# Performance work log

Measured on AMD Instinct MI355X. Metric: run time of the kernel, lower is better.

## Reference

```python
import jax, jax.numpy as jnp
import numpy as np

N_NODES = 100000
N_EDGES = 3200000
IN_DIM = 20
HIDDEN = 4096
OUT_DIM = 2
BN_EPS = 1e-5


def setup_inputs() -> dict:
    key = jax.random.key(0)
    ks = jax.random.split(key, 6)
    node_feature = jax.random.normal(ks[0], (N_NODES, IN_DIM), dtype=jnp.float32)
    edge_index = jax.random.randint(ks[1], (2, N_EDGES), 0, N_NODES, dtype=jnp.int64)
    gcn_w = jax.random.normal(ks[2], (IN_DIM, HIDDEN), dtype=jnp.float32) * (1.0 / np.sqrt(IN_DIM))
    gcn_b = jax.random.normal(ks[3], (HIDDEN,), dtype=jnp.float32) * 0.01
    bn_gamma = jnp.ones((HIDDEN,), dtype=jnp.float32)
    bn_beta = jnp.zeros((HIDDEN,), dtype=jnp.float32)
    lin_w = jax.random.normal(ks[4], (HIDDEN, OUT_DIM), dtype=jnp.float32) * (1.0 / np.sqrt(HIDDEN))
    lin_b = jnp.zeros((OUT_DIM,), dtype=jnp.float32)
    return {"node_feature": node_feature, "edge_index": edge_index,
            "gcn_w": gcn_w, "gcn_b": gcn_b, "bn_gamma": bn_gamma,
            "bn_beta": bn_beta, "lin_w": lin_w, "lin_b": lin_b}


def reference(node_feature, edge_index, gcn_w, gcn_b, bn_gamma, bn_beta, lin_w, lin_b):
    n = node_feature.shape[0]
    # --- GCNConv: add self loops, symmetric degree normalization ---
    loop = jnp.arange(n, dtype=edge_index.dtype)
    row = jnp.concatenate([edge_index[0], loop])  # source nodes
    col = jnp.concatenate([edge_index[1], loop])  # destination nodes
    deg = jax.ops.segment_sum(jnp.ones(col.shape[0], dtype=node_feature.dtype), col, num_segments=n)
    dinv = jnp.where(deg > 0, jax.lax.rsqrt(deg), 0.0)
    norm = dinv[row] * dinv[col]  # [E+N]
    # Aggregate in the small input dim (20), then transform: scatter(norm*x)W == scatter(norm*xW)
    msgs = node_feature[row] * norm[:, None]              # [E+N, in]
    agg = jax.ops.segment_sum(msgs, col, num_segments=n)  # [N, in]
    h = agg @ gcn_w + gcn_b                                # [N, hidden]
    # --- BatchNorm1d (training-mode batch stats, biased variance) ---
    mean = jnp.mean(h, axis=0)
    var = jnp.mean(jnp.square(h - mean), axis=0)
    h = (h - mean) * jax.lax.rsqrt(var + BN_EPS) * bn_gamma + bn_beta
    rsu_embedding = h[0:1]  # [1, hidden]
    # --- Linear -> ReLU -> Softmax(dim=1) ---
    logits = jax.nn.relu(h @ lin_w + lin_b)  # [N, out]
    action_prob = jax.nn.softmax(logits, axis=1)
    return action_prob, rsu_embedding
```

## Files before the change

kernel.cpp:

```cpp
#include <hip/hip_runtime.h>

#define N_NODES 100000
#define N_EDGES 3200000
#define IN_DIM 20
#define HIDDEN 4096
#define OUT_DIM 2
#define BN_EPS 1e-5f

#define NB 1000
#define NPB 100
#define BIN_CHUNK 8192
#define BIN_NWG ((N_EDGES + BIN_CHUNK - 1) / BIN_CHUNK)

#define WS_NEED 34415616ull

__global__ void k_deg(const int* __restrict__ ei, int* __restrict__ deg) {
    int e = blockIdx.x * blockDim.x + threadIdx.x;
    if (e < N_EDGES) atomicAdd(&deg[ei[N_EDGES + e]], 1);
}

__global__ void k_dinv(const int* __restrict__ deg, float* __restrict__ dinv) {
    int i = blockIdx.x * blockDim.x + threadIdx.x;
    if (i < N_NODES) dinv[i] = rsqrtf((float)(deg[i] + 1));
}

__global__ void k_bh(const int* __restrict__ deg, int* __restrict__ bh) {
    __shared__ int lds[128];
    int b = blockIdx.x, t = threadIdx.x;
    int v = (t < NPB) ? deg[b * NPB + t] : 0;
    lds[t] = v;
    __syncthreads();
    for (int off = 64; off > 0; off >>= 1) {
        if (t < off) lds[t] += lds[t + off];
        __syncthreads();
    }
    if (t == 0) bh[b] = lds[0];
}

__global__ void k_scan_bo(const int* __restrict__ bh, int* __restrict__ bo,
                          int* __restrict__ gcur) {
    __shared__ int lds[256];
    int t = threadIdx.x;
    int base = t * 4;
    int v0 = (base + 0 < NB) ? bh[base + 0] : 0;
    int v1 = (base + 1 < NB) ? bh[base + 1] : 0;
    int v2 = (base + 2 < NB) ? bh[base + 2] : 0;
    int v3 = (base + 3 < NB) ? bh[base + 3] : 0;
    int tsum = v0 + v1 + v2 + v3;
    int x = tsum;
    lds[t] = x;
    __syncthreads();
    for (int off = 1; off < 256; off <<= 1) {
        int y = (t >= off) ? lds[t - off] : 0;
        __syncthreads();
        x += y;
        lds[t] = x;
        __syncthreads();
    }
    int ex = x - tsum;
    if (base + 0 < NB) { bo[base + 0] = ex;                 gcur[base + 0] = ex; }
    if (base + 1 < NB) { bo[base + 1] = ex + v0;            gcur[base + 1] = ex + v0; }
    if (base + 2 < NB) { bo[base + 2] = ex + v0 + v1;       gcur[base + 2] = ex + v0 + v1; }
    if (base + 3 < NB) { bo[base + 3] = ex + v0 + v1 + v2;  gcur[base + 3] = ex + v0 + v1 + v2; }
    if (t == 255) bo[NB] = x;
}

__global__ void k_bin(const int* __restrict__ ei, int* __restrict__ gcur,
                      int2* __restrict__ rec) {
    __shared__ int lh[NB];
    __shared__ int loff[NB];
    int t = threadIdx.x;
    int ebase = blockIdx.x * BIN_CHUNK;
    int eend = min(ebase + BIN_CHUNK, N_EDGES);
    for (int b = t; b < NB; b += 256) lh[b] = 0;
    __syncthreads();
    for (int e = ebase + t; e < eend; e += 256) {
        int c = ei[N_EDGES + e];
        atomicAdd(&lh[c / NPB], 1);
    }
    __syncthreads();
    for (int b = t; b < NB; b += 256) {
        int cnt = lh[b];
        loff[b] = cnt ? atomicAdd(&gcur[b], cnt) : 0;
        lh[b] = 0;
    }
    __syncthreads();
    for (int e = ebase + t; e < eend; e += 256) {
        int r = ei[e];
        int c = ei[N_EDGES + e];
        int b = c / NPB;
        int p = loff[b] + atomicAdd(&lh[b], 1);
        rec[p] = make_int2(r, c);
    }
}

__global__ void k_agg(const int2* __restrict__ rec, const int* __restrict__ bo,
                      const float* __restrict__ nf, const float* __restrict__ dinv,
                      float* __restrict__ agg) {
    __shared__ float tile[NPB * IN_DIM];
    __shared__ float sdinv[NPB];
    int b = blockIdx.x;
    int t = threadIdx.x;
    int base = b * NPB;
    if (t < NPB) sdinv[t] = dinv[base + t];
    __syncthreads();
    const float4* nf4 = (const float4*)nf;
    float4* tile4 = (float4*)tile;
    for (int idx = t; idx < NPB * IN_DIM / 4; idx += 256) {
        int j = idx / 5;
        float d = sdinv[j];
        float s = d * d;
        float4 v = nf4[base * 5 + idx];
        v.x *= s; v.y *= s; v.z *= s; v.w *= s;
        tile4[idx] = v;
    }
    __syncthreads();
    int rend = bo[b + 1];
    for (int i = bo[b] + t; i < rend; i += 256) {
        int2 rc = rec[i];
        int r = rc.x;
        int cl = rc.y - base;
        float w = dinv[r] * sdinv[cl];
        const float4* nfr = nf4 + r * 5;
        float* dst = tile + cl * IN_DIM;
#pragma unroll
        for (int g = 0; g < 5; g++) {
            float4 v = nfr[g];
            atomicAdd(&dst[g * 4 + 0], v.x * w);
            atomicAdd(&dst[g * 4 + 1], v.y * w);
            atomicAdd(&dst[g * 4 + 2], v.z * w);
            atomicAdd(&dst[g * 4 + 3], v.w * w);
        }
    }
    __syncthreads();
    float4* agg4 = (float4*)agg;
    for (int idx = t; idx < NPB * IN_DIM / 4; idx += 256)
        agg4[base * 5 + idx] = tile4[idx];
}

__global__ void k_moments3(const float* __restrict__ agg, float* __restrict__ S1,
                           float* __restrict__ S2) {
    int y = blockIdx.y;
    int a0 = 3 * y, a1 = 3 * y + 1, a2 = 3 * y + 2;
    float acc0[IN_DIM], acc1[IN_DIM], acc2[IN_DIM];
#pragma unroll
    for (int b = 0; b < IN_DIM; b++) { acc0[b] = 0.f; acc1[b] = 0.f; acc2[b] = 0.f; }
    int stride = gridDim.x * blockDim.x;
    for (int i = blockIdx.x * blockDim.x + threadIdx.x; i < N_NODES; i += stride) {
        const float* row = agg + i * IN_DIM;
        float v[IN_DIM];
#pragma unroll
        for (int b = 0; b < IN_DIM; b++) v[b] = row[b];
        float va0 = row[a0];
        float va1 = row[a1];
        float va2 = (a2 < IN_DIM) ? row[a2] : 1.0f;
#pragma unroll
        for (int b = 0; b < IN_DIM; b++) {
            acc0[b] += va0 * v[b];
            acc1[b] += va1 * v[b];
            acc2[b] += va2 * v[b];
        }
    }
#pragma unroll
    for (int b = 0; b < IN_DIM; b++) {
        float r0 = acc0[b], r1 = acc1[b], r2 = acc2[b];
#pragma unroll
        for (int s = 32; s > 0; s >>= 1) {
            r0 += __shfl_down(r0, s);
            r1 += __shfl_down(r1, s);
            r2 += __shfl_down(r2, s);
        }
        acc0[b] = r0; acc1[b] = r1; acc2[b] = r2;
    }
    if ((threadIdx.x & 63) == 0) {
        float* d0 = S2 + a0 * IN_DIM;
        float* d1 = S2 + a1 * IN_DIM;
        float* d2 = (a2 < IN_DIM) ? (S2 + a2 * IN_DIM) : S1;
#pragma unroll
        for (int b = 0; b < IN_DIM; b++) {
            atomicAdd(&d0[b], acc0[b]);
            atomicAdd(&d1[b], acc1[b]);
            atomicAdd(&d2[b], acc2[b]);
        }
    }
}

__global__ void k_stats(const float* __restrict__ S1, const float* __restrict__ S2,
                        const float* __restrict__ agg, float* __restrict__ mean,
                        float* __restrict__ cov, float* __restrict__ agg0c) {
    int t = threadIdx.x;
    const float invn = 1.0f / (float)N_NODES;
    if (t < IN_DIM) {
        float m = S1[t] * invn;
        mean[t] = m;
        agg0c[t] = agg[t] - m;
    }
    __syncthreads();
    for (int idx = t; idx < IN_DIM * IN_DIM; idx += 64) {
        int a = idx / IN_DIM, b = idx - a * IN_DIM;
        cov[idx] = S2[idx] * invn - mean[a] * mean[b];
    }
}

__global__ void k_prep(const float* __restrict__ gcn_w, const float* __restrict__ gamma,
                       const float* __restrict__ beta, const float* __restrict__ lin_w,
                       const float* __restrict__ cov, const float* __restrict__ agg0c,
                       float* __restrict__ W2, float* __restrict__ dvec,
                       float* __restrict__ out_rsu) {
    __shared__ float scov[IN_DIM * IN_DIM];
    __shared__ float sa0[IN_DIM];
    int tid = threadIdx.x;
    for (int idx = tid; idx < IN_DIM * IN_DIM; idx += blockDim.x) scov[idx] = cov[idx];
    if (tid < IN_DIM) sa0[tid] = agg0c[tid];
    __syncthreads();
    int j = blockIdx.x * blockDim.x + tid;

    float wcol[IN_DIM];
#pragma unroll
    for (int t = 0; t < IN_DIM; t++) wcol[t] = gcn_w[t * HIDDEN + j];

    float var = 0.f;
#pragma unroll
    for (int t = 0; t < IN_DIM; t++) {
        float s = 0.f;
#pragma unroll
        for (int u = 0; u < IN_DIM; u++) s += scov[t * IN_DIM + u] * wcol[u];
        var += wcol[t] * s;
    }
    float aj = gamma[j] * rsqrtf(var + BN_EPS);

    float e0 = 0.f;
#pragma unroll
    for (int t = 0; t < IN_DIM; t++) e0 += sa0[t] * wcol[t];
    out_rsu[j] = e0 * aj + beta[j];

    float lw0 = lin_w[2 * j], lw1 = lin_w[2 * j + 1];
    float bj = beta[j];
    float vals[42];
#pragma unroll
    for (int t = 0; t < IN_DIM; t++) {
        vals[2 * t]     = wcol[t] * aj * lw0;
        vals[2 * t + 1] = wcol[t] * aj * lw1;
    }
    vals[40] = bj * lw0;
    vals[41] = bj * lw1;
#pragma unroll
    for (int q = 0; q < 42; q++) {
        float v = vals[q];
#pragma unroll
        for (int s = 32; s > 0; s >>= 1) v += __shfl_down(v, s);
        if ((tid & 63) == 0) {
            if (q < 40) atomicAdd(&W2[q], v);
            else        atomicAdd(&dvec[q - 40], v);
        }
    }
}

__global__ void k_final(const float* __restrict__ agg, const float* __restrict__ mean,
                        const float* __restrict__ W2, const float* __restrict__ dvec,
                        const float* __restrict__ lin_b, float* __restrict__ out) {
    int i = blockIdx.x * blockDim.x + threadIdx.x;
    if (i >= N_NODES) return;
    float d0 = dvec[0] + lin_b[0];
    float d1 = dvec[1] + lin_b[1];
#pragma unroll
    for (int t = 0; t < IN_DIM; t++) {
        float v = agg[i * IN_DIM + t] - mean[t];
        d0 += v * W2[2 * t];
        d1 += v * W2[2 * t + 1];
    }
    float l0 = fmaxf(d0, 0.f), l1 = fmaxf(d1, 0.f);
    float m = fmaxf(l0, l1);
    float e0 = expf(l0 - m), e1 = expf(l1 - m);
    float inv = 1.f / (e0 + e1);
    out[2 * i]     = e0 * inv;
    out[2 * i + 1] = e1 * inv;
}

__global__ void k_agginit(const float* __restrict__ nf, const float* __restrict__ dinv,
                          float* __restrict__ agg) {
    int t = blockIdx.x * blockDim.x + threadIdx.x;
    if (t < N_NODES * IN_DIM) {
        int i = t / IN_DIM;
        float d = dinv[i];
        agg[t] = nf[t] * d * d;
    }
}

__global__ void k_scatter(const int* __restrict__ ei, const float* __restrict__ nf,
                          const float* __restrict__ dinv, float* __restrict__ agg) {
    int t = blockIdx.x * blockDim.x + threadIdx.x;
    if (t >= N_EDGES * IN_DIM) return;
    int e = t / IN_DIM;
    int f = t - e * IN_DIM;
    int r = ei[e];
    int c = ei[N_EDGES + e];
    float w = dinv[r] * dinv[c];
    atomicAdd(&agg[c * IN_DIM + f], nf[r * IN_DIM + f] * w);
}

extern "C" void kernel_launch(void* const* d_in, const int* in_sizes, int n_in,
                              void* d_out, int out_size, void* d_ws, size_t ws_size,
                              hipStream_t stream) {
    const float* nf    = (const float*)d_in[0];
    const int*   ei    = (const int*)d_in[1];
    const float* gcn_w = (const float*)d_in[2];
    const float* gamma = (const float*)d_in[4];
    const float* beta  = (const float*)d_in[5];
    const float* lin_w = (const float*)d_in[6];
    const float* lin_b = (const float*)d_in[7];
    float* out = (float*)d_out;

    char* ws = (char*)d_ws;
    int*   deg  = (int*)(ws + 0);
    float* dinv = (float*)(ws + 400000);
    float* agg  = (float*)(ws + 800000);
    int*   bh   = (int*)(ws + 8800000);
    int*   bo   = (int*)(ws + 8804000);
    int*   gcur = (int*)(ws + 8808004);
    float* S1   = (float*)(ws + 8812004);
    float* S2   = (float*)(ws + 8812084);
    float* mean = (float*)(ws + 8813684);
    float* cov  = (float*)(ws + 8813764);
    float* a0c  = (float*)(ws + 8815364);
    float* W2   = (float*)(ws + 8815444);
    float* dvec = (float*)(ws + 8815604);
    int2*  rec  = (int2*)(ws + 8815616);

    hipMemsetAsync(deg, 0, 400000, stream);
    hipMemsetAsync(S1, 0, 3608, stream);

    k_deg<<<(N_EDGES + 255) / 256, 256, 0, stream>>>(ei, deg);
    k_dinv<<<(N_NODES + 255) / 256, 256, 0, stream>>>(deg, dinv);

    if (ws_size >= WS_NEED) {
        k_bh<<<NB, 128, 0, stream>>>(deg, bh);
        k_scan_bo<<<1, 256, 0, stream>>>(bh, bo, gcur);
        k_bin<<<BIN_NWG, 256, 0, stream>>>(ei, gcur, rec);
        k_agg<<<NB, 256, 0, stream>>>(rec, bo, nf, dinv, agg);
    } else {
        k_agginit<<<(N_NODES * IN_DIM + 255) / 256, 256, 0, stream>>>(nf, dinv, agg);
        k_scatter<<<(N_EDGES * IN_DIM + 255) / 256, 256, 0, stream>>>(ei, nf, dinv, agg);
    }

    dim3 gm(32, 7);
    k_moments3<<<gm, 256, 0, stream>>>(agg, S1, S2);
    k_stats<<<1, 64, 0, stream>>>(S1, S2, agg, mean, cov, a0c);
    k_prep<<<HIDDEN / 256, 256, 0, stream>>>(gcn_w, gamma, beta, lin_w, cov, a0c, W2,
                                             dvec, out + 2 * N_NODES);
    k_final<<<(N_NODES + 255) / 256, 256, 0, stream>>>(agg, mean, W2, dvec, lin_b, out);
}
```

Baseline: 704.9 us.

## Prescale node features by dinv, pack edge records, enlarge agg/bin blocks

Adds a kernel that writes node features pre-multiplied by their source dinv, so the aggregation no longer gathers dinv[r] per edge. The post-sum multiply by the destination dinv moves to the write-out. Edge records shrink from int2 to a packed 32-bit value (source<<7 | local column), which halves record traffic in binning and aggregation. Block sizes for bin and agg grow, and the moments grid is widened. The cost is an extra pass over the features and extra workspace.

```diff
diff --git a/kernel.cpp b/kernel.cpp
--- a/kernel.cpp
+++ b/kernel.cpp
@@ -10,9 +10,11 @@
 #define NB 1000
 #define NPB 100
 #define BIN_CHUNK 8192
+#define BIN_THREADS 512
 #define BIN_NWG ((N_EDGES + BIN_CHUNK - 1) / BIN_CHUNK)
-
-#define WS_NEED 34415616ull
+#define AGG_THREADS 1024
+
+#define WS_NEED 29615616ull
 
 __global__ void k_deg(const int* __restrict__ ei, int* __restrict__ deg) {
     int e = blockIdx.x * blockDim.x + threadIdx.x;
@@ -22,6 +24,21 @@
 __global__ void k_dinv(const int* __restrict__ deg, float* __restrict__ dinv) {
     int i = blockIdx.x * blockDim.x + threadIdx.x;
     if (i < N_NODES) dinv[i] = rsqrtf((float)(deg[i] + 1));
+}
+
+__global__ void k_nfs(const float* __restrict__ nf, const float* __restrict__ dinv,
+                      float* __restrict__ nfs) {
+    int i = blockIdx.x * blockDim.x + threadIdx.x;
+    if (i >= N_NODES) return;
+    float d = dinv[i];
+    const float4* s = (const float4*)nf + i * 5;
+    float4* o = (float4*)nfs + i * 5;
+#pragma unroll
+    for (int g = 0; g < 5; g++) {
+        float4 v = s[g];
+        v.x *= d; v.y *= d; v.z *= d; v.w *= d;
+        o[g] = v;
+    }
 }
 
 __global__ void k_bh(const int* __restrict__ deg, int* __restrict__ bh) {
@@ -66,36 +83,34 @@
 }
 
 __global__ void k_bin(const int* __restrict__ ei, int* __restrict__ gcur,
-                      int2* __restrict__ rec) {
+                      unsigned int* __restrict__ rec) {
     __shared__ int lh[NB];
     __shared__ int loff[NB];
     int t = threadIdx.x;
     int ebase = blockIdx.x * BIN_CHUNK;
     int eend = min(ebase + BIN_CHUNK, N_EDGES);
-    for (int b = t; b < NB; b += 256) lh[b] = 0;
-    __syncthreads();
-    for (int e = ebase + t; e < eend; e += 256) {
-        int c = ei[N_EDGES + e];
-        atomicAdd(&lh[c / NPB], 1);
-    }
-    __syncthreads();
-    for (int b = t; b < NB; b += 256) {
+    for (int b = t; b < NB; b += BIN_THREADS) lh[b] = 0;
+    __syncthreads();
+    for (int e = ebase + t; e < eend; e += BIN_THREADS)
+        atomicAdd(&lh[ei[N_EDGES + e] / NPB], 1);
+    __syncthreads();
+    for (int b = t; b < NB; b += BIN_THREADS) {
         int cnt = lh[b];
         loff[b] = cnt ? atomicAdd(&gcur[b], cnt) : 0;
         lh[b] = 0;
     }
     __syncthreads();
-    for (int e = ebase + t; e < eend; e += 256) {
+    for (int e = ebase + t; e < eend; e += BIN_THREADS) {
         int r = ei[e];
         int c = ei[N_EDGES + e];
         int b = c / NPB;
         int p = loff[b] + atomicAdd(&lh[b], 1);
-        rec[p] = make_int2(r, c);
-    }
-}
-
-__global__ void k_agg(const int2* __restrict__ rec, const int* __restrict__ bo,
-                      const float* __restrict__ nf, const float* __restrict__ dinv,
+        rec[p] = ((unsigned int)r << 7) | (unsigned int)(c - b * NPB);
+    }
+}
+
+__global__ void k_agg(const unsigned int* __restrict__ rec, const int* __restrict__ bo,
+                      const float* __restrict__ nfs, const float* __restrict__ dinv,
                       float* __restrict__ agg) {
     __shared__ float tile[NPB * IN_DIM];
     __shared__ float sdinv[NPB];
@@ -103,39 +118,36 @@
     int t = threadIdx.x;
     int base = b * NPB;
     if (t < NPB) sdinv[t] = dinv[base + t];
-    __syncthreads();
-    const float4* nf4 = (const float4*)nf;
+    const float4* nfs4 = (const float4*)nfs;
     float4* tile4 = (float4*)tile;
-    for (int idx = t; idx < NPB * IN_DIM / 4; idx += 256) {
+    for (int idx = t; idx < NPB * IN_DIM / 4; idx += AGG_THREADS)
+        tile4[idx] = nfs4[base * 5 + idx];
+    __syncthreads();
+    int rend = bo[b + 1];
+    for (int i = bo[b] + t; i < rend; i += AGG_THREADS) {
+        unsigned int v = rec[i];
+        int r = (int)(v >> 7);
+        int cl = (int)(v & 127u);
+        const float4* nfr = nfs4 + r * 5;
+        float* dst = tile + cl * IN_DIM;
+#pragma unroll
+        for (int g = 0; g < 5; g++) {
+            float4 x = nfr[g];
+            atomicAdd(&dst[g * 4 + 0], x.x);
+            atomicAdd(&dst[g * 4 + 1], x.y);
+            atomicAdd(&dst[g * 4 + 2], x.z);
+            atomicAdd(&dst[g * 4 + 3], x.w);
+        }
+    }
+    __syncthreads();
+    float4* agg4 = (float4*)agg;
+    for (int idx = t; idx < NPB * IN_DIM / 4; idx += AGG_THREADS) {
         int j = idx / 5;
-        float d = sdinv[j];
-        float s = d * d;
-        float4 v = nf4[base * 5 + idx];
-        v.x *= s; v.y *= s; v.z *= s; v.w *= s;
-        tile4[idx] = v;
-    }
-    __syncthreads();
-    int rend = bo[b + 1];
-    for (int i = bo[b] + t; i < rend; i += 256) {
-        int2 rc = rec[i];
-        int r = rc.x;
-        int cl = rc.y - base;
-        float w = dinv[r] * sdinv[cl];
-        const float4* nfr = nf4 + r * 5;
-        float* dst = tile + cl * IN_DIM;
-#pragma unroll
-        for (int g = 0; g < 5; g++) {
-            float4 v = nfr[g];
-            atomicAdd(&dst[g * 4 + 0], v.x * w);
-            atomicAdd(&dst[g * 4 + 1], v.y * w);
-            atomicAdd(&dst[g * 4 + 2], v.z * w);
-            atomicAdd(&dst[g * 4 + 3], v.w * w);
-        }
-    }
-    __syncthreads();
-    float4* agg4 = (float4*)agg;
-    for (int idx = t; idx < NPB * IN_DIM / 4; idx += 256)
-        agg4[base * 5 + idx] = tile4[idx];
+        float s = sdinv[j];
+        float4 x = tile4[idx];
+        x.x *= s; x.y *= s; x.z *= s; x.w *= s;
+        agg4[base * 5 + idx] = x;
+    }
 }
 
 __global__ void k_moments3(const float* __restrict__ agg, float* __restrict__ S1,
@@ -325,7 +337,8 @@
     float* a0c  = (float*)(ws + 8815364);
     float* W2   = (float*)(ws + 8815444);
     float* dvec = (float*)(ws + 8815604);
-    int2*  rec  = (int2*)(ws + 8815616);
+    unsigned int* rec = (unsigned int*)(ws + 8815616);
+    float* nfs  = (float*)(ws + 21615616);
 
     hipMemsetAsync(deg, 0, 400000, stream);
     hipMemsetAsync(S1, 0, 3608, stream);
@@ -334,16 +347,17 @@
     k_dinv<<<(N_NODES + 255) / 256, 256, 0, stream>>>(deg, dinv);
 
     if (ws_size >= WS_NEED) {
+        k_nfs<<<(N_NODES + 255) / 256, 256, 0, stream>>>(nf, dinv, nfs);
         k_bh<<<NB, 128, 0, stream>>>(deg, bh);
         k_scan_bo<<<1, 256, 0, stream>>>(bh, bo, gcur);
-        k_bin<<<BIN_NWG, 256, 0, stream>>>(ei, gcur, rec);
-        k_agg<<<NB, 256, 0, stream>>>(rec, bo, nf, dinv, agg);
+        k_bin<<<BIN_NWG, BIN_THREADS, 0, stream>>>(ei, gcur, rec);
+        k_agg<<<NB, AGG_THREADS, 0, stream>>>(rec, bo, nfs, dinv, agg);
     } else {
         k_agginit<<<(N_NODES * IN_DIM + 255) / 256, 256, 0, stream>>>(nf, dinv, agg);
         k_scatter<<<(N_EDGES * IN_DIM + 255) / 256, 256, 0, stream>>>(ei, nf, dinv, agg);
     }
 
-    dim3 gm(32, 7);
+    dim3 gm(128, 7);
     k_moments3<<<gm, 256, 0, stream>>>(agg, S1, S2);
     k_stats<<<1, 64, 0, stream>>>(S1, S2, agg, mean, cov, a0c);
     k_prep<<<HIDDEN / 256, 256, 0, stream>>>(gcn_w, gamma, beta, lin_w, cov, a0c, W2,
```

Result: slower. 963.0 us (+36.6%).
